# Performance work log

Measured on AMD Instinct MI355X. Metric: run time of the kernel, lower is better.

## Reference

```python
import jax, jax.numpy as jnp
import numpy as np
from jax import lax

B, S, L = 128, 256, 10
WORD, CHAR = 50000, 100
TAGS, START, END = 32, 30, 31
WDIM, CDIM, FILT, H = 100, 30, 30, 100
LSTM_IN = WDIM + FILT  # 130
NEG = -10000.0


def setup_inputs() -> dict:
    key = jax.random.key(0)
    ks = jax.random.split(key, 24)
    sc = 0.1
    word_emb = (jax.random.normal(ks[0], (WORD, WDIM), jnp.float32) * sc).at[0].set(0.0)  # padding_idx=0
    char_emb = (jax.random.normal(ks[1], (CHAR, CDIM), jnp.float32) * sc).at[0].set(0.0)
    conv_w = jax.random.normal(ks[2], (FILT, 1, 3, CDIM), jnp.float32) * sc  # OIHW, kernel (3, char_dim)
    conv_b = jax.random.normal(ks[3], (FILT,), jnp.float32) * sc
    wih_f = jax.random.normal(ks[4], (4 * H, LSTM_IN), jnp.float32) * sc
    whh_f = jax.random.normal(ks[5], (4 * H, H), jnp.float32) * sc
    bih_f = jax.random.normal(ks[6], (4 * H,), jnp.float32) * sc
    bhh_f = jax.random.normal(ks[7], (4 * H,), jnp.float32) * sc
    wih_b = jax.random.normal(ks[8], (4 * H, LSTM_IN), jnp.float32) * sc
    whh_b = jax.random.normal(ks[9], (4 * H, H), jnp.float32) * sc
    bih_b = jax.random.normal(ks[10], (4 * H,), jnp.float32) * sc
    bhh_b = jax.random.normal(ks[11], (4 * H,), jnp.float32) * sc
    proj_w = jax.random.normal(ks[12], (TAGS, 2 * H), jnp.float32) * sc
    proj_b = jax.random.normal(ks[13], (TAGS,), jnp.float32) * sc
    trans = jax.random.normal(ks[14], (TAGS, TAGS), jnp.float32)
    trans = trans.at[:, START].set(NEG).at[END, :].set(NEG)  # CRF.reset_parm
    word_x = jax.random.randint(ks[15], (B, S), 1, WORD, jnp.int32)
    char_x = jax.random.randint(ks[16], (B, S, L), 1, CHAR, jnp.int32)
    y = jax.random.randint(ks[17], (B, S), 0, 30, jnp.int32)  # gold tags exclude start/end
    mask = jnp.ones((B, S), jnp.int32)
    return dict(word_emb=word_emb, char_emb=char_emb, conv_w=conv_w, conv_b=conv_b,
                wih_f=wih_f, whh_f=whh_f, bih_f=bih_f, bhh_f=bhh_f,
                wih_b=wih_b, whh_b=whh_b, bih_b=bih_b, bhh_b=bhh_b,
                proj_w=proj_w, proj_b=proj_b, trans=trans,
                word_x=word_x, char_x=char_x, y=y, mask=mask)


def _lstm_dir(x, wih, whh, bih, bhh, reverse):
    # x: [B, S, D] -> hidden states [B, S, H]; PyTorch gate order i, f, g, o
    b = bih + bhh
    xs = jnp.swapaxes(x, 0, 1)  # [S, B, D]
    if reverse:
        xs = xs[::-1]
    Bv = x.shape[0]
    Hd = whh.shape[1]
    init = (jnp.zeros((Bv, Hd), x.dtype), jnp.zeros((Bv, Hd), x.dtype))
    def step(carry, xt):
        h, c = carry
        g = xt @ wih.T + h @ whh.T + b  # [B, 4H]
        i, f, gg, o = jnp.split(g, 4, axis=-1)
        c = jax.nn.sigmoid(f) * c + jax.nn.sigmoid(i) * jnp.tanh(gg)
        h = jax.nn.sigmoid(o) * jnp.tanh(c)
        return (h, c), h
    _, hs = lax.scan(step, init, xs)
    if reverse:
        hs = hs[::-1]
    return jnp.swapaxes(hs, 0, 1)


def _forward(word_emb, char_emb, conv_w, conv_b, wih_f, whh_f, bih_f, bhh_f,
             wih_b, whh_b, bih_b, bhh_b, proj_w, proj_b, trans,
             word_x, char_x, y, mask):
    # --- CharCNN (dropout = identity in eval) ---
    ce = char_emb[char_x].reshape(B * S, 1, L, CDIM)  # [B*S, 1, L, CDIM]
    fm = lax.conv_general_dilated(ce, conv_w, (1, 1), ((2, 2), (0, 0)),
                                  dimension_numbers=('NCHW', 'OIHW', 'NCHW'))
    fm = fm + conv_b[None, :, None, None]  # [B*S, FILT, L+2, 1]
    char_feat = fm.max(axis=(2, 3)).reshape(B, S, FILT)
    # --- BiLSTM + projection ---
    x = jnp.concatenate([word_emb[word_x], char_feat], axis=-1)  # [B, S, 130]
    h_f = _lstm_dir(x, wih_f, whh_f, bih_f, bhh_f, False)
    h_b = _lstm_dir(x, wih_b, whh_b, bih_b, bhh_b, True)
    emission = jnp.concatenate([h_f, h_b], axis=-1) @ proj_w.T + proj_b  # [B, S, TAGS]
    maskf = mask.astype(emission.dtype)
    # --- CRF gold-path score (vectorized form of compute_y_score) ---
    y_pad = jnp.concatenate([jnp.full((B, 1), START, y.dtype), y], axis=1)  # [B, S+1]
    prev, cur = y_pad[:, :-1], y_pad[:, 1:]
    p = jnp.take_along_axis(emission, cur[..., None].astype(jnp.int32), axis=-1)[..., 0]
    t = trans[prev, cur]
    score_y = ((p + t) * maskf).sum(axis=1) + trans[y[:, -1], END]  # original uses last label unmasked
    # --- CRF partition function (logsumexp scan over time) ---
    la0 = jnp.full((B, TAGS), NEG, emission.dtype).at[:, START].set(0.0)
    def step(la, em_m):
        em, m = em_m  # em: [B, TAGS], m: [B]
        la2 = jax.nn.logsumexp(la[:, :, None] + trans[None, :, :] + em[:, None, :], axis=1)
        m = m[:, None]
        return la2 * m + la * (1.0 - m), None
    la, _ = lax.scan(step, la0, (jnp.swapaxes(emission, 0, 1), maskf.T))
    la = la + trans[:, END][None, :]
    total = jax.nn.logsumexp(la, axis=1, keepdims=True)  # [B, 1]
    # faithful to original: [B] - [B,1] broadcasts to [B,B], then mean
    return -jnp.mean(score_y - total)


def reference(word_emb, char_emb, conv_w, conv_b, wih_f, whh_f, bih_f, bhh_f,
              wih_b, whh_b, bih_b, bhh_b, proj_w, proj_b, trans,
              word_x, char_x, y, mask):
    return _forward(word_emb, char_emb, conv_w, conv_b, wih_f, whh_f, bih_f, bhh_f,
                    wih_b, whh_b, bih_b, bhh_b, proj_w, proj_b, trans,
                    word_x, char_x, y, mask)
```

## Files before the change

kernel.cpp:

```cpp
#include <hip/hip_runtime.h>
#include <hip/hip_fp16.h>
#include <cstdint>
#include <cstddef>

#define BB 128
#define SS 256
#define LL 10
#define NTAGS 32
#define TAG_START 30
#define TAG_END 31
#define WDIM 100
#define CDIM 30
#define NFILT 30
#define HDIM 100
#define KIN 130
#define KPAD 160
#define GDIM 400
#define NROWS 832
#define NEGV -10000.0f
#define CTOK 8

#define NB_CONV (BB * SS / CTOK)
#define NB_WORDA (BB * SS * 12 / 256)
#define NB_WORDB (BB * SS * 20 / 256)
#define NB_WCVT (NROWS * KPAD / 256)
#define NB_PRE  (NB_CONV + NB_WORDA + NB_WORDB + NB_WCVT)

typedef _Float16 h2 __attribute__((ext_vector_type(2)));
typedef _Float16 f16x8 __attribute__((ext_vector_type(8)));
typedef float f32x4 __attribute__((ext_vector_type(4)));

__device__ __forceinline__ float sigm(float x) { return 1.0f / (1.0f + __expf(-x)); }
__device__ __forceinline__ float tanh_fast(float x) { return 2.0f / (1.0f + __expf(-2.0f * x)) - 1.0f; }

__device__ __forceinline__ void barrier_lds_only() {
  asm volatile("s_waitcnt lgkmcnt(0)" ::: "memory");
  __builtin_amdgcn_s_barrier();
  asm volatile("" ::: "memory");
}

__global__ __launch_bounds__(256) void k_pre(
    const float* __restrict__ wemb, const int* __restrict__ wx,
    const float* __restrict__ cemb, const float* __restrict__ convw,
    const float* __restrict__ convb, const int* __restrict__ cx,
    const float* __restrict__ wihF, const float* __restrict__ wihB,
    _Float16* __restrict__ x16, _Float16* __restrict__ w16,
    float* __restrict__ out) {
  int blk = blockIdx.x;
  int tid = threadIdx.x;
  if (blk == 0 && tid == 0) out[0] = 0.f;

  if (blk < NB_CONV) {
    int tok8 = tid >> 5;
    int f = tid & 31;
    int token0 = blk * CTOK;
    __shared__ float e[CTOK][LL * CDIM];
    __shared__ float cw[NFILT * 3 * CDIM];
    __shared__ float cb[NFILT];
    __shared__ int ci[CTOK][LL];
    if (tid < CTOK * LL) {
      int t = tid / LL, l = tid - t * LL;
      ci[t][l] = cx[(token0 + t) * LL + l];
    }
    for (int i = tid; i < NFILT * 3 * CDIM; i += 256) cw[i] = convw[i];
    if (tid < NFILT) cb[tid] = convb[tid];
    __syncthreads();
    for (int i = tid; i < CTOK * LL * CDIM; i += 256) {
      int t = i / (LL * CDIM);
      int r = i - t * (LL * CDIM);
      int l = r / CDIM, c = r - l * CDIM;
      e[t][l * CDIM + c] = cemb[ci[t][l] * CDIM + c];
    }
    __syncthreads();
    if (f < NFILT) {
      float d0[LL], d1[LL], d2[LL];
#pragma unroll
      for (int l = 0; l < LL; l++) { d0[l] = 0.f; d1[l] = 0.f; d2[l] = 0.f; }
      const float* et = &e[tok8][0];
      for (int c = 0; c < CDIM; c++) {
        float w0 = cw[(f * 3 + 0) * CDIM + c];
        float w1 = cw[(f * 3 + 1) * CDIM + c];
        float w2 = cw[(f * 3 + 2) * CDIM + c];
#pragma unroll
        for (int l = 0; l < LL; l++) {
          float ev = et[l * CDIM + c];
          d0[l] += ev * w0; d1[l] += ev * w1; d2[l] += ev * w2;
        }
      }
      float bias = cb[f];
      float m = -3.0e38f;
#pragma unroll
      for (int h = 0; h < LL + 2; h++) {
        float acc = bias;
        int j0 = h - 2, j1 = h - 1, j2 = h;
        if (j0 >= 0 && j0 < LL) acc += d0[j0];
        if (j1 >= 0 && j1 < LL) acc += d1[j1];
        if (j2 >= 0 && j2 < LL) acc += d2[j2];
        m = fmaxf(m, acc);
      }
      x16[(size_t)(token0 + tok8) * KPAD + WDIM + f] = (_Float16)m;
    }
  } else if (blk < NB_CONV + NB_WORDA) {
    int idx = (blk - NB_CONV) * 256 + tid;
    int token = idx / 12;
    int g = idx - token * 12;
    const float* src = wemb + (size_t)wx[token] * WDIM + g * 8;
    float4 f0 = *(const float4*)(src);
    float4 f1 = *(const float4*)(src + 4);
    f16x8 v;
    v[0] = (_Float16)f0.x; v[1] = (_Float16)f0.y;
    v[2] = (_Float16)f0.z; v[3] = (_Float16)f0.w;
    v[4] = (_Float16)f1.x; v[5] = (_Float16)f1.y;
    v[6] = (_Float16)f1.z; v[7] = (_Float16)f1.w;
    *(f16x8*)&x16[(size_t)token * KPAD + g * 8] = v;
  } else if (blk < NB_CONV + NB_WORDA + NB_WORDB) {
    int idx = (blk - NB_CONV - NB_WORDA) * 256 + tid;
    int token = idx / 20;
    int u = idx - token * 20;
    if (u < 4) {
      x16[(size_t)token * KPAD + 96 + u] = (_Float16)wemb[(size_t)wx[token] * WDIM + 96 + u];
    } else if (u < 19) {
      *(uint32_t*)&x16[(size_t)token * KPAD + KIN + 2 * (u - 4)] = 0;
    }
  } else {
    int idx = (blk - NB_CONV - NB_WORDA - NB_WORDB) * 256 + tid;
    int n = idx / KPAD;
    int k = idx - n * KPAD;
    float v = 0.f;
    if (k < KIN && n < 2 * GDIM) {
      v = (n < GDIM) ? wihF[(size_t)n * KIN + k] : wihB[(size_t)(n - GDIM) * KIN + k];
    }
    w16[idx] = (_Float16)v;
  }
}

__global__ __launch_bounds__(256) void k_pregemm(
    const _Float16* __restrict__ x16, const _Float16* __restrict__ w16,
    const float* __restrict__ bihF, const float* __restrict__ bhhF,
    const float* __restrict__ bihB, const float* __restrict__ bhhB,
    _Float16* __restrict__ preF, _Float16* __restrict__ preB) {
  __shared__ __align__(16) _Float16 Asl[64 * 168];
  __shared__ __align__(16) _Float16 Bsl[2][64 * 168];
  int m0 = blockIdx.x * 64;
  int tid = threadIdx.x;
  int lane = tid & 63, w = tid >> 6;
  int quad = lane >> 4, l15 = lane & 15;
  int r = tid >> 2;
  int kk = (tid & 3) * 8;

  const _Float16* xs = x16 + (size_t)(m0 + r) * KPAD + kk;
  const _Float16* ws = w16 + (size_t)r * KPAD + kk;
#pragma unroll
  for (int kc = 0; kc < 5; kc++) {
    *(f16x8*)&Asl[r * 168 + kc * 32 + kk] = *(const f16x8*)(xs + kc * 32);
    *(f16x8*)&Bsl[0][r * 168 + kc * 32 + kk] = *(const f16x8*)(ws + kc * 32);
  }
  __syncthreads();

  for (int nt = 0; nt < 13; nt++) {
    int cur = nt & 1;
    f16x8 nb0, nb1, nb2, nb3, nb4;
    if (nt + 1 < 13) {
      const _Float16* wn = w16 + (size_t)((nt + 1) * 64 + r) * KPAD + kk;
      nb0 = *(const f16x8*)(wn);
      nb1 = *(const f16x8*)(wn + 32);
      nb2 = *(const f16x8*)(wn + 64);
      nb3 = *(const f16x8*)(wn + 96);
      nb4 = *(const f16x8*)(wn + 128);
    }

    f32x4 acc[4];
#pragma unroll
    for (int i = 0; i < 4; i++) acc[i] = (f32x4){0.f, 0.f, 0.f, 0.f};
#pragma unroll
    for (int kc = 0; kc < 5; kc++) {
      f16x8 bfrag = *(const f16x8*)&Bsl[cur][(w * 16 + l15) * 168 + kc * 32 + quad * 8];
#pragma unroll
      for (int mt = 0; mt < 4; mt++) {
        f16x8 afrag = *(const f16x8*)&Asl[(mt * 16 + l15) * 168 + kc * 32 + quad * 8];
        acc[mt] = __builtin_amdgcn_mfma_f32_16x16x32_f16(afrag, bfrag, acc[mt], 0, 0, 0);
      }
    }

    int ng = nt * 64 + w * 16 + l15;
    if (ng < 2 * GDIM) {
      int dir = ng >= GDIM;
      int jb = dir ? ng - GDIM : ng;
      _Float16* dst = dir ? preB : preF;
      float bias = (dir ? bihB : bihF)[jb] + (dir ? bhhB : bhhF)[jb];
#pragma unroll
      for (int mt = 0; mt < 4; mt++) {
#pragma unroll
        for (int i = 0; i < 4; i++) {
          int m = m0 + mt * 16 + quad * 4 + i;
          dst[(size_t)m * GDIM + jb] = (_Float16)(acc[mt][i] + bias);
        }
      }
    }

    if (nt + 1 < 13) {
      asm volatile("s_waitcnt vmcnt(0)" ::: "memory");
      int nxt = cur ^ 1;
      *(f16x8*)&Bsl[nxt][r * 168 + 0 * 32 + kk] = nb0;
      *(f16x8*)&Bsl[nxt][r * 168 + 1 * 32 + kk] = nb1;
      *(f16x8*)&Bsl[nxt][r * 168 + 2 * 32 + kk] = nb2;
      *(f16x8*)&Bsl[nxt][r * 168 + 3 * 32 + kk] = nb3;
      *(f16x8*)&Bsl[nxt][r * 168 + 4 * 32 + kk] = nb4;
      __syncthreads();
    }
  }
}

#define CH 32
#define NCH (SS / CH)
__global__ __launch_bounds__(256, 1) void k_lstm(
    const _Float16* __restrict__ preF, const _Float16* __restrict__ preB,
    const float* __restrict__ whhF, const float* __restrict__ whhB,
    _Float16* __restrict__ hbuf) {
  int blk = blockIdx.x;
  int dir = blk >> 7;
  int b = blk & 127;
  const _Float16* pre = dir ? preB : preF;
  const float* whh = dir ? whhB : whhF;
  int tid = threadIdx.x;
  int j = tid >> 1;
  int kh = tid & 1;
  bool act = (j < HDIM);
  int jc = act ? j : 0;

  __half2 wp[4][25];
#pragma unroll
  for (int g = 0; g < 4; g++) {
    const float* wr = whh + (size_t)(g * HDIM + jc) * HDIM + kh * 50;
#pragma unroll
    for (int q = 0; q < 25; q++) {
      wp[g][q] = __floats2half2_rn(wr[2 * q], wr[2 * q + 1]);
    }
  }

  __shared__ __align__(16) _Float16 preS[14336];
  __shared__ __align__(16) _Float16 hsh[2][2][64];
  if (tid < 128) ((int*)hsh)[tid] = 0;
  float c = 0.f;

#define GSRC(ck) ((const uint4*)(pre + ((size_t)b * SS + (dir ? (SS - CH - (ck) * CH) : ((ck) * CH))) * GDIM))

  uint4 r0, r1, r2, r3, r4, r5, r6;
  {
    const uint4* s0 = GSRC(0);
    r0 = s0[0 * 256 + tid]; r1 = s0[1 * 256 + tid]; r2 = s0[2 * 256 + tid];
    r3 = s0[3 * 256 + tid]; r4 = s0[4 * 256 + tid]; r5 = s0[5 * 256 + tid];
    r6 = s0[6 * 256 + tid];
  }

  _Float16* hptr = hbuf + ((size_t)b * SS + (dir ? (SS - 1) : 0)) * (2 * HDIM) + dir * HDIM + jc;
  const intptr_t hstep = dir ? -(intptr_t)(2 * HDIM) : (intptr_t)(2 * HDIM);

  int cur = 0;
  for (int ck = 0; ck < NCH; ck++) {
    asm volatile("s_waitcnt vmcnt(0)" ::: "memory");
    *(uint4*)&preS[(0 * 256 + tid) * 8] = r0;
    *(uint4*)&preS[(1 * 256 + tid) * 8] = r1;
    *(uint4*)&preS[(2 * 256 + tid) * 8] = r2;
    *(uint4*)&preS[(3 * 256 + tid) * 8] = r3;
    *(uint4*)&preS[(4 * 256 + tid) * 8] = r4;
    *(uint4*)&preS[(5 * 256 + tid) * 8] = r5;
    *(uint4*)&preS[(6 * 256 + tid) * 8] = r6;
    if (ck + 1 < NCH) {
      const uint4* snx = GSRC(ck + 1);
      r0 = snx[0 * 256 + tid]; r1 = snx[1 * 256 + tid]; r2 = snx[2 * 256 + tid];
      r3 = snx[3 * 256 + tid]; r4 = snx[4 * 256 + tid]; r5 = snx[5 * 256 + tid];
      r6 = snx[6 * 256 + tid];
    }
    barrier_lds_only();

    int preOff = (dir ? (CH - 1) * GDIM : 0) + kh * 200 + jc;
    const int pdelta = dir ? -GDIM : GDIM;

    for (int s2 = 0; s2 < CH; s2++) {
      float paF = (float)preS[preOff];
      float pbF = (float)preS[preOff + 100];

      const _Float16* hseg = &hsh[cur][kh][0];
      uint4 hv0 = *(const uint4*)(hseg);
      uint4 hv1 = *(const uint4*)(hseg + 8);
      uint4 hv2 = *(const uint4*)(hseg + 16);
      uint4 hv3 = *(const uint4*)(hseg + 24);
      uint4 hv4 = *(const uint4*)(hseg + 32);
      uint4 hv5 = *(const uint4*)(hseg + 40);
      uint32_t hv6 = *(const uint32_t*)(hseg + 48);
      __half2 hp[25];
      hp[0]  = __builtin_bit_cast(__half2, hv0.x);
      hp[1]  = __builtin_bit_cast(__half2, hv0.y);
      hp[2]  = __builtin_bit_cast(__half2, hv0.z);
      hp[3]  = __builtin_bit_cast(__half2, hv0.w);
      hp[4]  = __builtin_bit_cast(__half2, hv1.x);
      hp[5]  = __builtin_bit_cast(__half2, hv1.y);
      hp[6]  = __builtin_bit_cast(__half2, hv1.z);
      hp[7]  = __builtin_bit_cast(__half2, hv1.w);
      hp[8]  = __builtin_bit_cast(__half2, hv2.x);
      hp[9]  = __builtin_bit_cast(__half2, hv2.y);
      hp[10] = __builtin_bit_cast(__half2, hv2.z);
      hp[11] = __builtin_bit_cast(__half2, hv2.w);
      hp[12] = __builtin_bit_cast(__half2, hv3.x);
      hp[13] = __builtin_bit_cast(__half2, hv3.y);
      hp[14] = __builtin_bit_cast(__half2, hv3.z);
      hp[15] = __builtin_bit_cast(__half2, hv3.w);
      hp[16] = __builtin_bit_cast(__half2, hv4.x);
      hp[17] = __builtin_bit_cast(__half2, hv4.y);
      hp[18] = __builtin_bit_cast(__half2, hv4.z);
      hp[19] = __builtin_bit_cast(__half2, hv4.w);
      hp[20] = __builtin_bit_cast(__half2, hv5.x);
      hp[21] = __builtin_bit_cast(__half2, hv5.y);
      hp[22] = __builtin_bit_cast(__half2, hv5.z);
      hp[23] = __builtin_bit_cast(__half2, hv5.w);
      hp[24] = __builtin_bit_cast(__half2, hv6);

      float racc[4];
      __half2 z = __floats2half2_rn(0.f, 0.f);
#pragma unroll
      for (int g = 0; g < 4; g++) {
        __half2 a0 = z, a1 = z;
#pragma unroll
        for (int q = 0; q < 25; q += 2) a0 = __hfma2(wp[g][q], hp[q], a0);
#pragma unroll
        for (int q = 1; q < 25; q += 2) a1 = __hfma2(wp[g][q], hp[q], a1);
        racc[g] = (__low2float(a0) + __high2float(a0)) +
                  (__low2float(a1) + __high2float(a1));
      }

      if (kh == 0) { racc[0] += paF; racc[1] += pbF; }
      else         { racc[2] += paF; racc[3] += pbF; }
#pragma unroll
      for (int g = 0; g < 4; g++) racc[g] += __shfl_xor(racc[g], 1);

      float ig = sigm(racc[0]), fg = sigm(racc[1]);
      float g2 = tanh_fast(racc[2]), og = sigm(racc[3]);
      c = fg * c + ig * g2;
      float h = og * tanh_fast(c);

      if (act && kh == 0) {
        int seg = (j >= 50) ? 1 : 0;
        hsh[cur ^ 1][seg][j - seg * 50] = (_Float16)h;
        *hptr = (_Float16)h;
      }

      barrier_lds_only();
      cur ^= 1;
      preOff += pdelta;
      hptr += hstep;
    }
  }
#undef GSRC
}

__global__ __launch_bounds__(256) void k_proj(const _Float16* __restrict__ hbuf,
                                              const float* __restrict__ pw,
                                              const float* __restrict__ pb,
                                              float* __restrict__ em) {
  __shared__ __align__(16) float pws[NTAGS * 204];
  __shared__ float pbs[NTAGS];
  int tid = threadIdx.x;
  for (int i = tid; i < NTAGS * 2 * HDIM; i += 256) {
    int tag = i / (2 * HDIM);
    int k = i - tag * (2 * HDIM);
    pws[tag * 204 + k] = pw[i];
  }
  if (tid < NTAGS) pbs[tid] = pb[tid];
  __syncthreads();

  int idx = blockIdx.x * blockDim.x + tid;
  if (idx >= BB * SS * NTAGS) return;
  int token = idx >> 5, tag = idx & 31;
  const uint4* h4 = (const uint4*)(hbuf + (size_t)token * 2 * HDIM);
  const float4* w4 = (const float4*)&pws[tag * 204];
  float acc = pbs[tag];
#pragma unroll
  for (int k = 0; k < 25; k++) {
    uint4 hv = h4[k];
    h2 a = __builtin_bit_cast(h2, hv.x);
    h2 bq = __builtin_bit_cast(h2, hv.y);
    h2 cq = __builtin_bit_cast(h2, hv.z);
    h2 d = __builtin_bit_cast(h2, hv.w);
    float4 w0 = w4[k * 2], w1 = w4[k * 2 + 1];
    acc += (float)a.x * w0.x + (float)a.y * w0.y + (float)bq.x * w0.z + (float)bq.y * w0.w
         + (float)cq.x * w1.x + (float)cq.y * w1.y + (float)d.x * w1.z + (float)d.y * w1.w;
  }
  em[idx] = acc;
}

__global__ __launch_bounds__(64) void k_crf(const float* __restrict__ em,
                                            const float* __restrict__ trans,
                                            const int* __restrict__ mask,
                                            const int* __restrict__ y,
                                            float* __restrict__ out) {
  int b = blockIdx.x;
  int lane = threadIdx.x;
  int j = lane & 31;
  int h = lane >> 5;

  __shared__ __align__(16) float emS[SS * NTAGS];
  __shared__ __align__(16) int mkS[SS];
  __shared__ __align__(16) float laS[2][32];
  {
    const uint4* src = (const uint4*)(em + (size_t)b * SS * NTAGS);
#pragma unroll
    for (int p = 0; p < 32; p++) {
      uint4 t = src[p * 64 + lane];
      *(uint4*)&emS[(p * 64 + lane) * 4] = t;
    }
    uint4 mv = ((const uint4*)(mask + (size_t)b * SS))[lane];
    *(uint4*)&mkS[lane * 4] = mv;
  }
  barrier_lds_only();

  float sacc = 0.f;
  for (int s = lane; s < SS; s += 64) {
    int curt = y[b * SS + s];
    int prevt = (s == 0) ? TAG_START : y[b * SS + s - 1];
    float mk = (float)mkS[s];
    sacc += (emS[s * NTAGS + curt] + trans[prevt * NTAGS + curt]) * mk;
  }
#pragma unroll
  for (int off = 32; off > 0; off >>= 1) sacc += __shfl_down(sacc, off);
  float scoreYv = __shfl(sacc, 0) + trans[y[b * SS + SS - 1] * NTAGS + TAG_END];

  float tcol[16];
#pragma unroll
  for (int i = 0; i < 16; i++) tcol[i] = trans[(h * 16 + i) * NTAGS + j];

  float la = (j == TAG_START) ? 0.f : NEGV;

  for (int s = 0; s < SS; s++) {
    float e0 = emS[s * NTAGS + j];
    float mkv = (float)mkS[s];

    if (lane < 32) laS[s & 1][lane] = la;
    asm volatile("s_waitcnt lgkmcnt(0)" ::: "memory");
    const float4* lp = (const float4*)&laS[s & 1][h * 16];
    float4 t0 = lp[0], t1 = lp[1], t2 = lp[2], t3 = lp[3];

    float v[16];
    v[0] = t0.x + tcol[0];  v[1] = t0.y + tcol[1];
    v[2] = t0.z + tcol[2];  v[3] = t0.w + tcol[3];
    v[4] = t1.x + tcol[4];  v[5] = t1.y + tcol[5];
    v[6] = t1.z + tcol[6];  v[7] = t1.w + tcol[7];
    v[8] = t2.x + tcol[8];  v[9] = t2.y + tcol[9];
    v[10] = t2.z + tcol[10]; v[11] = t2.w + tcol[11];
    v[12] = t3.x + tcol[12]; v[13] = t3.y + tcol[13];
    v[14] = t3.z + tcol[14]; v[15] = t3.w + tcol[15];

    float ma = v[0], mb2 = v[1];
#pragma unroll
    for (int i = 2; i < 16; i += 2) { ma = fmaxf(ma, v[i]); mb2 = fmaxf(mb2, v[i + 1]); }
    float mh = fmaxf(ma, mb2);
    float m = fmaxf(mh, __shfl_xor(mh, 32));

    float sa = 0.f, sb = 0.f;
#pragma unroll
    for (int i = 0; i < 16; i += 2) { sa += __expf(v[i] - m); sb += __expf(v[i + 1] - m); }
    float sh = sa + sb;
    float sum = sh + __shfl_xor(sh, 32);

    float la2 = m + __logf(sum) + e0;
    la = la2 * mkv + la * (1.f - mkv);
  }
  la += trans[j * NTAGS + TAG_END];

  float mm = la;
#pragma unroll
  for (int off = 16; off > 0; off >>= 1) mm = fmaxf(mm, __shfl_xor(mm, off));
  float ss = __expf(la - mm);
#pragma unroll
  for (int off = 16; off > 0; off >>= 1) ss += __shfl_xor(ss, off);
  float total = mm + __logf(ss);
  if (lane == 0) atomicAdd(out, (total - scoreYv) * (1.0f / BB));
}

extern "C" void kernel_launch(void* const* d_in, const int* in_sizes, int n_in,
                              void* d_out, int out_size, void* d_ws, size_t ws_size,
                              hipStream_t stream) {
  const float* word_emb = (const float*)d_in[0];
  const float* char_emb = (const float*)d_in[1];
  const float* conv_w   = (const float*)d_in[2];
  const float* conv_b   = (const float*)d_in[3];
  const float* wih_f    = (const float*)d_in[4];
  const float* whh_f    = (const float*)d_in[5];
  const float* bih_f    = (const float*)d_in[6];
  const float* bhh_f    = (const float*)d_in[7];
  const float* wih_b    = (const float*)d_in[8];
  const float* whh_b    = (const float*)d_in[9];
  const float* bih_b    = (const float*)d_in[10];
  const float* bhh_b    = (const float*)d_in[11];
  const float* proj_w   = (const float*)d_in[12];
  const float* proj_b   = (const float*)d_in[13];
  const float* trans    = (const float*)d_in[14];
  const int* word_x     = (const int*)d_in[15];
  const int* char_x     = (const int*)d_in[16];
  const int* y          = (const int*)d_in[17];
  const int* mask       = (const int*)d_in[18];
  float* out = (float*)d_out;

  _Float16* x16   = (_Float16*)d_ws;
  _Float16* w16   = x16 + (size_t)BB * SS * KPAD;
  _Float16* preF  = w16 + (size_t)NROWS * KPAD;
  _Float16* preB  = preF + (size_t)BB * SS * GDIM;
  _Float16* hbuf  = preB + (size_t)BB * SS * GDIM;
  float* em       = (float*)(hbuf + (size_t)BB * SS * 2 * HDIM);

  k_pre<<<NB_PRE, 256, 0, stream>>>(word_emb, word_x, char_emb, conv_w, conv_b,
                                    char_x, wih_f, wih_b, x16, w16, out);
  k_pregemm<<<BB * SS / 64, 256, 0, stream>>>(x16, w16, bih_f, bhh_f,
                                              bih_b, bhh_b, preF, preB);
  k_lstm<<<256, 256, 0, stream>>>(preF, preB, whh_f, whh_b, hbuf);
  k_proj<<<(BB * SS * NTAGS + 255) / 256, 256, 0, stream>>>(hbuf, proj_w, proj_b, em);
  k_crf<<<BB, 64, 0, stream>>>(em, trans, mask, y, out);
}
```

Before: 483.4 us.

## Fuse projection into CRF kernel and use fdot2 in LSTM recurrence

The tag projection is folded into the CRF kernel, so each of the 128 blocks computes its own sequence's emissions straight into LDS. This removes the separate projection launch and the global round trip of the emission buffer. The LSTM inner dot products switch to the fdot2 builtin, which accumulates in fp32 instead of chaining half2 FMAs, cutting instructions and improving precision. The risk is that the projection now runs on only 128 blocks instead of thousands, which may lengthen it, and the extra shared memory lowers occupancy.

Measured after the change: 563.5 us. 16.6% more time.

```diff
diff --git a/kernel.cpp b/kernel.cpp
--- a/kernel.cpp
+++ b/kernel.cpp
@@ -29,6 +29,12 @@
 typedef _Float16 h2 __attribute__((ext_vector_type(2)));
 typedef _Float16 f16x8 __attribute__((ext_vector_type(8)));
 typedef float f32x4 __attribute__((ext_vector_type(4)));
+
+#if __has_builtin(__builtin_amdgcn_fdot2)
+#define HAVE_FDOT2 1
+#else
+#define HAVE_FDOT2 0
+#endif
 
 __device__ __forceinline__ float sigm(float x) { return 1.0f / (1.0f + __expf(-x)); }
 __device__ __forceinline__ float tanh_fast(float x) { return 2.0f / (1.0f + __expf(-2.0f * x)) - 1.0f; }
@@ -317,6 +323,21 @@
       hp[24] = __builtin_bit_cast(__half2, hv6);
 
       float racc[4];
+#if HAVE_FDOT2
+#pragma unroll
+      for (int g = 0; g < 4; g++) {
+        float a0 = 0.f, a1 = 0.f;
+#pragma unroll
+        for (int q = 0; q < 25; q += 2)
+          a0 = __builtin_amdgcn_fdot2(__builtin_bit_cast(h2, wp[g][q]),
+                                      __builtin_bit_cast(h2, hp[q]), a0, false);
+#pragma unroll
+        for (int q = 1; q < 25; q += 2)
+          a1 = __builtin_amdgcn_fdot2(__builtin_bit_cast(h2, wp[g][q]),
+                                      __builtin_bit_cast(h2, hp[q]), a1, false);
+        racc[g] = a0 + a1;
+      }
+#else
       __half2 z = __floats2half2_rn(0.f, 0.f);
 #pragma unroll
       for (int g = 0; g < 4; g++) {
@@ -328,6 +349,7 @@
         racc[g] = (__low2float(a0) + __high2float(a0)) +
                   (__low2float(a1) + __high2float(a1));
       }
+#endif
 
       if (kh == 0) { racc[0] += paF; racc[1] += pbF; }
       else         { racc[2] += paF; racc[3] += pbF; }
@@ -354,65 +376,62 @@
 #undef GSRC
 }
 
-__global__ __launch_bounds__(256) void k_proj(const _Float16* __restrict__ hbuf,
-                                              const float* __restrict__ pw,
-                                              const float* __restrict__ pb,
-                                              float* __restrict__ em) {
+__global__ __launch_bounds__(256) void k_crf(const _Float16* __restrict__ hbuf,
+                                             const float* __restrict__ pw,
+                                             const float* __restrict__ pb,
+                                             const float* __restrict__ trans,
+                                             const int* __restrict__ mask,
+                                             const int* __restrict__ y,
+                                             float* __restrict__ out) {
+  int b = blockIdx.x;
+  int tid = threadIdx.x;
+
+  __shared__ __align__(16) float emS[SS * NTAGS];
   __shared__ __align__(16) float pws[NTAGS * 204];
   __shared__ float pbs[NTAGS];
-  int tid = threadIdx.x;
+  __shared__ __align__(16) int mkS[SS];
+  __shared__ __align__(16) float laS[2][32];
+
   for (int i = tid; i < NTAGS * 2 * HDIM; i += 256) {
-    int tag = i / (2 * HDIM);
-    int k = i - tag * (2 * HDIM);
-    pws[tag * 204 + k] = pw[i];
+    int tg = i / (2 * HDIM);
+    int k = i - tg * (2 * HDIM);
+    pws[tg * 204 + k] = pw[i];
   }
   if (tid < NTAGS) pbs[tid] = pb[tid];
+  if (tid < 64) {
+    uint4 mv = ((const uint4*)(mask + (size_t)b * SS))[tid];
+    *(uint4*)&mkS[tid * 4] = mv;
+  }
   __syncthreads();
 
-  int idx = blockIdx.x * blockDim.x + tid;
-  if (idx >= BB * SS * NTAGS) return;
-  int token = idx >> 5, tag = idx & 31;
-  const uint4* h4 = (const uint4*)(hbuf + (size_t)token * 2 * HDIM);
-  const float4* w4 = (const float4*)&pws[tag * 204];
-  float acc = pbs[tag];
-#pragma unroll
-  for (int k = 0; k < 25; k++) {
-    uint4 hv = h4[k];
-    h2 a = __builtin_bit_cast(h2, hv.x);
-    h2 bq = __builtin_bit_cast(h2, hv.y);
-    h2 cq = __builtin_bit_cast(h2, hv.z);
-    h2 d = __builtin_bit_cast(h2, hv.w);
-    float4 w0 = w4[k * 2], w1 = w4[k * 2 + 1];
-    acc += (float)a.x * w0.x + (float)a.y * w0.y + (float)bq.x * w0.z + (float)bq.y * w0.w
-         + (float)cq.x * w1.x + (float)cq.y * w1.y + (float)d.x * w1.z + (float)d.y * w1.w;
-  }
-  em[idx] = acc;
-}
-
-__global__ __launch_bounds__(64) void k_crf(const float* __restrict__ em,
-                                            const float* __restrict__ trans,
-                                            const int* __restrict__ mask,
-                                            const int* __restrict__ y,
-                                            float* __restrict__ out) {
-  int b = blockIdx.x;
-  int lane = threadIdx.x;
+  {
+    int tag = tid & 31;
+    int tok8 = tid >> 5;
+    const float4* w4 = (const float4*)&pws[tag * 204];
+    for (int it = 0; it < 32; it++) {
+      int token = it * 8 + tok8;
+      const uint4* h4 = (const uint4*)(hbuf + ((size_t)b * SS + token) * 2 * HDIM);
+      float acc = pbs[tag];
+#pragma unroll
+      for (int k = 0; k < 25; k++) {
+        uint4 hv = h4[k];
+        h2 a = __builtin_bit_cast(h2, hv.x);
+        h2 bq = __builtin_bit_cast(h2, hv.y);
+        h2 cq = __builtin_bit_cast(h2, hv.z);
+        h2 d = __builtin_bit_cast(h2, hv.w);
+        float4 w0 = w4[k * 2], w1 = w4[k * 2 + 1];
+        acc += (float)a.x * w0.x + (float)a.y * w0.y + (float)bq.x * w0.z + (float)bq.y * w0.w
+             + (float)cq.x * w1.x + (float)cq.y * w1.y + (float)d.x * w1.z + (float)d.y * w1.w;
+      }
+      emS[token * NTAGS + tag] = acc;
+    }
+  }
+  barrier_lds_only();
+
+  if (tid >= 64) return;
+  int lane = tid;
   int j = lane & 31;
   int h = lane >> 5;
-
-  __shared__ __align__(16) float emS[SS * NTAGS];
-  __shared__ __align__(16) int mkS[SS];
-  __shared__ __align__(16) float laS[2][32];
-  {
-    const uint4* src = (const uint4*)(em + (size_t)b * SS * NTAGS);
-#pragma unroll
-    for (int p = 0; p < 32; p++) {
-      uint4 t = src[p * 64 + lane];
-      *(uint4*)&emS[(p * 64 + lane) * 4] = t;
-    }
-    uint4 mv = ((const uint4*)(mask + (size_t)b * SS))[lane];
-    *(uint4*)&mkS[lane * 4] = mv;
-  }
-  barrier_lds_only();
 
   float sacc = 0.f;
   for (int s = lane; s < SS; s += 64) {
@@ -506,13 +525,11 @@
   _Float16* preF  = w16 + (size_t)NROWS * KPAD;
   _Float16* preB  = preF + (size_t)BB * SS * GDIM;
   _Float16* hbuf  = preB + (size_t)BB * SS * GDIM;
-  float* em       = (float*)(hbuf + (size_t)BB * SS * 2 * HDIM);
 
   k_pre<<<NB_PRE, 256, 0, stream>>>(word_emb, word_x, char_emb, conv_w, conv_b,
                                     char_x, wih_f, wih_b, x16, w16, out);
   k_pregemm<<<BB * SS / 64, 256, 0, stream>>>(x16, w16, bih_f, bhh_f,
                                               bih_b, bhh_b, preF, preB);
   k_lstm<<<256, 256, 0, stream>>>(preF, preB, whh_f, whh_b, hbuf);
-  k_proj<<<(BB * SS * NTAGS + 255) / 256, 256, 0, stream>>>(hbuf, proj_w, proj_b, em);
-  k_crf<<<BB, 64, 0, stream>>>(em, trans, mask, y, out);
+  k_crf<<<BB, 256, 0, stream>>>(hbuf, proj_w, proj_b, trans, mask, y, out);
 }
```

## Use fdot2 in LSTM recurrence and stream CRF emissions with packed waves

Applied to the files above, without the earlier changes.

The LSTM hidden-state dot products now use the fdot2 builtin, which accumulates f16 pairs into f32, instead of half2 FMA chains followed by a horizontal sum. This cuts instructions and raises accumulation precision. The CRF kernel packs 16 batch rows into one 1024-thread block, one wave per row. It double-buffers 8-step emission chunks through LDS with a prefetch, replacing the upfront 32KB per-row copy and the block barrier. The gold-path score now reads emissions from global memory, and with only 8 blocks the CRF may leave most CUs idle.

Measured after the change: 590.1 us. +22.1%, slower.

```diff
diff --git a/kernel.cpp b/kernel.cpp
--- a/kernel.cpp
+++ b/kernel.cpp
@@ -29,6 +29,12 @@
 typedef _Float16 h2 __attribute__((ext_vector_type(2)));
 typedef _Float16 f16x8 __attribute__((ext_vector_type(8)));
 typedef float f32x4 __attribute__((ext_vector_type(4)));
+
+#if __has_builtin(__builtin_amdgcn_fdot2)
+#define HAVE_FDOT2 1
+#else
+#define HAVE_FDOT2 0
+#endif
 
 __device__ __forceinline__ float sigm(float x) { return 1.0f / (1.0f + __expf(-x)); }
 __device__ __forceinline__ float tanh_fast(float x) { return 2.0f / (1.0f + __expf(-2.0f * x)) - 1.0f; }
@@ -317,6 +323,21 @@
       hp[24] = __builtin_bit_cast(__half2, hv6);
 
       float racc[4];
+#if HAVE_FDOT2
+#pragma unroll
+      for (int g = 0; g < 4; g++) {
+        float a0 = 0.f, a1 = 0.f;
+#pragma unroll
+        for (int q = 0; q < 25; q += 2)
+          a0 = __builtin_amdgcn_fdot2(__builtin_bit_cast(h2, wp[g][q]),
+                                      __builtin_bit_cast(h2, hp[q]), a0, false);
+#pragma unroll
+        for (int q = 1; q < 25; q += 2)
+          a1 = __builtin_amdgcn_fdot2(__builtin_bit_cast(h2, wp[g][q]),
+                                      __builtin_bit_cast(h2, hp[q]), a1, false);
+        racc[g] = a0 + a1;
+      }
+#else
       __half2 z = __floats2half2_rn(0.f, 0.f);
 #pragma unroll
       for (int g = 0; g < 4; g++) {
@@ -328,6 +349,7 @@
         racc[g] = (__low2float(a0) + __high2float(a0)) +
                   (__low2float(a1) + __high2float(a1));
       }
+#endif
 
       if (kh == 0) { racc[0] += paF; racc[1] += pbF; }
       else         { racc[2] += paF; racc[3] += pbF; }
@@ -389,37 +411,38 @@
   em[idx] = acc;
 }
 
-__global__ __launch_bounds__(64) void k_crf(const float* __restrict__ em,
-                                            const float* __restrict__ trans,
-                                            const int* __restrict__ mask,
-                                            const int* __restrict__ y,
-                                            float* __restrict__ out) {
-  int b = blockIdx.x;
-  int lane = threadIdx.x;
+#define CRF_W 16
+#define CRF_CH 8
+__global__ __launch_bounds__(1024, 1) void k_crf(const float* __restrict__ em,
+                                                 const float* __restrict__ trans,
+                                                 const int* __restrict__ mask,
+                                                 const int* __restrict__ y,
+                                                 float* __restrict__ out) {
+  int tid = threadIdx.x;
+  int w = tid >> 6;
+  int lane = tid & 63;
+  int b = blockIdx.x * CRF_W + w;
   int j = lane & 31;
   int h = lane >> 5;
 
-  __shared__ __align__(16) float emS[SS * NTAGS];
-  __shared__ __align__(16) int mkS[SS];
-  __shared__ __align__(16) float laS[2][32];
+  __shared__ __align__(16) float emS[CRF_W][2][CRF_CH * 32];
+  __shared__ __align__(16) int mkS[CRF_W][SS];
+  __shared__ __align__(16) float laS[CRF_W][2][32];
+
   {
-    const uint4* src = (const uint4*)(em + (size_t)b * SS * NTAGS);
-#pragma unroll
-    for (int p = 0; p < 32; p++) {
-      uint4 t = src[p * 64 + lane];
-      *(uint4*)&emS[(p * 64 + lane) * 4] = t;
-    }
     uint4 mv = ((const uint4*)(mask + (size_t)b * SS))[lane];
-    *(uint4*)&mkS[lane * 4] = mv;
-  }
-  barrier_lds_only();
+    *(uint4*)&mkS[w][lane * 4] = mv;
+  }
+  asm volatile("s_waitcnt lgkmcnt(0)" ::: "memory");
+
+  const float* emb_g = em + (size_t)b * SS * NTAGS;
 
   float sacc = 0.f;
   for (int s = lane; s < SS; s += 64) {
     int curt = y[b * SS + s];
     int prevt = (s == 0) ? TAG_START : y[b * SS + s - 1];
-    float mk = (float)mkS[s];
-    sacc += (emS[s * NTAGS + curt] + trans[prevt * NTAGS + curt]) * mk;
+    float mk = (float)mkS[w][s];
+    sacc += (emb_g[s * NTAGS + curt] + trans[prevt * NTAGS + curt]) * mk;
   }
 #pragma unroll
   for (int off = 32; off > 0; off >>= 1) sacc += __shfl_down(sacc, off);
@@ -431,39 +454,52 @@
 
   float la = (j == TAG_START) ? 0.f : NEGV;
 
-  for (int s = 0; s < SS; s++) {
-    float e0 = emS[s * NTAGS + j];
-    float mkv = (float)mkS[s];
-
-    if (lane < 32) laS[s & 1][lane] = la;
-    asm volatile("s_waitcnt lgkmcnt(0)" ::: "memory");
-    const float4* lp = (const float4*)&laS[s & 1][h * 16];
-    float4 t0 = lp[0], t1 = lp[1], t2 = lp[2], t3 = lp[3];
-
-    float v[16];
-    v[0] = t0.x + tcol[0];  v[1] = t0.y + tcol[1];
-    v[2] = t0.z + tcol[2];  v[3] = t0.w + tcol[3];
-    v[4] = t1.x + tcol[4];  v[5] = t1.y + tcol[5];
-    v[6] = t1.z + tcol[6];  v[7] = t1.w + tcol[7];
-    v[8] = t2.x + tcol[8];  v[9] = t2.y + tcol[9];
-    v[10] = t2.z + tcol[10]; v[11] = t2.w + tcol[11];
-    v[12] = t3.x + tcol[12]; v[13] = t3.y + tcol[13];
-    v[14] = t3.z + tcol[14]; v[15] = t3.w + tcol[15];
-
-    float ma = v[0], mb2 = v[1];
-#pragma unroll
-    for (int i = 2; i < 16; i += 2) { ma = fmaxf(ma, v[i]); mb2 = fmaxf(mb2, v[i + 1]); }
-    float mh = fmaxf(ma, mb2);
-    float m = fmaxf(mh, __shfl_xor(mh, 32));
-
-    float sa = 0.f, sb = 0.f;
-#pragma unroll
-    for (int i = 0; i < 16; i += 2) { sa += __expf(v[i] - m); sb += __expf(v[i + 1] - m); }
-    float sh = sa + sb;
-    float sum = sh + __shfl_xor(sh, 32);
-
-    float la2 = m + __logf(sum) + e0;
-    la = la2 * mkv + la * (1.f - mkv);
+  float4 st = ((const float4*)emb_g)[lane];
+
+  int cur = 0;
+  for (int ck = 0; ck < SS / CRF_CH; ck++) {
+    asm volatile("s_waitcnt vmcnt(0)" ::: "memory");
+    *(float4*)&emS[w][cur][lane * 4] = st;
+    if (ck + 1 < SS / CRF_CH) {
+      st = ((const float4*)(emb_g + (ck + 1) * CRF_CH * 32))[lane];
+    }
+
+    for (int s2 = 0; s2 < CRF_CH; s2++) {
+      int s = ck * CRF_CH + s2;
+      float e0 = emS[w][cur][s2 * 32 + j];
+      float mkv = (float)mkS[w][s];
+
+      if (lane < 32) laS[w][s & 1][lane] = la;
+      asm volatile("s_waitcnt lgkmcnt(0)" ::: "memory");
+      const float4* lp = (const float4*)&laS[w][s & 1][h * 16];
+      float4 t0 = lp[0], t1 = lp[1], t2 = lp[2], t3 = lp[3];
+
+      float v[16];
+      v[0] = t0.x + tcol[0];  v[1] = t0.y + tcol[1];
+      v[2] = t0.z + tcol[2];  v[3] = t0.w + tcol[3];
+      v[4] = t1.x + tcol[4];  v[5] = t1.y + tcol[5];
+      v[6] = t1.z + tcol[6];  v[7] = t1.w + tcol[7];
+      v[8] = t2.x + tcol[8];  v[9] = t2.y + tcol[9];
+      v[10] = t2.z + tcol[10]; v[11] = t2.w + tcol[11];
+      v[12] = t3.x + tcol[12]; v[13] = t3.y + tcol[13];
+      v[14] = t3.z + tcol[14]; v[15] = t3.w + tcol[15];
+
+      float ma = v[0], mb2 = v[1];
+#pragma unroll
+      for (int i = 2; i < 16; i += 2) { ma = fmaxf(ma, v[i]); mb2 = fmaxf(mb2, v[i + 1]); }
+      float mh = fmaxf(ma, mb2);
+      float m = fmaxf(mh, __shfl_xor(mh, 32));
+
+      float sa = 0.f, sb = 0.f;
+#pragma unroll
+      for (int i = 0; i < 16; i += 2) { sa += __expf(v[i] - m); sb += __expf(v[i + 1] - m); }
+      float sh = sa + sb;
+      float sum = sh + __shfl_xor(sh, 32);
+
+      float la2 = m + __logf(sum) + e0;
+      la = la2 * mkv + la * (1.f - mkv);
+    }
+    cur ^= 1;
   }
   la += trans[j * NTAGS + TAG_END];
 
@@ -514,5 +550,5 @@
                                               bih_b, bhh_b, preF, preB);
   k_lstm<<<256, 256, 0, stream>>>(preF, preB, whh_f, whh_b, hbuf);
   k_proj<<<(BB * SS * NTAGS + 255) / 256, 256, 0, stream>>>(hbuf, proj_w, proj_b, em);
-  k_crf<<<BB, 64, 0, stream>>>(em, trans, mask, y, out);
-}
+  k_crf<<<BB / CRF_W, 1024, 0, stream>>>(em, trans, mask, y, out);
+}
```
